# Kernel tuning notes

Measured on AMD Instinct MI355X. Metric: run time of the kernel, lower is better.

The kernel has to match this reference:

```python
import jax, jax.numpy as jnp
import numpy as np
from jax import lax

B, T, D = 16, 1024, 512
L_ORDER, R_ORDER = 1, 1
THRESHOLD = 1.0
SMOOTH = 1.0
NOISE = 0.0
TAIL = 0.45


def setup_inputs() -> dict:
    key = jax.random.key(0)
    k1, k2, k3, k4, k5 = jax.random.split(key, 5)
    hidden = jax.random.normal(k1, (B, T, D), dtype=jnp.float32)
    mask = jnp.ones((B, 1, T), dtype=jnp.float32)
    conv_w = jax.random.normal(k2, (D, 1, L_ORDER + R_ORDER + 1), dtype=jnp.float32) * 0.05
    conv_b = jax.random.normal(k3, (D,), dtype=jnp.float32) * 0.05
    lin_w = jax.random.normal(k4, (D,), dtype=jnp.float32) * 0.05
    lin_b = jax.random.normal(k5, (1,), dtype=jnp.float32) * 0.05
    return {"hidden": hidden, "mask": mask, "conv_w": conv_w, "conv_b": conv_b,
            "lin_w": lin_w, "lin_b": lin_b}


def _cif(hidden, alphas, threshold):
    # hidden [B, T1, D], alphas [B, T1]
    b, t1, d = hidden.shape

    def step(carry, xs):
        integrate, frame = carry          # [B], [B, D]
        alpha, h_t = xs                   # [B], [B, D]
        dist = 1.0 - integrate
        integrate = integrate + alpha
        fires_t = integrate
        fire = integrate >= threshold
        integrate = jnp.where(fire, integrate - 1.0, integrate)
        cur = jnp.where(fire, dist, alpha)
        rem = alpha - cur
        frame = frame + cur[:, None] * h_t
        frames_t = frame
        frame = jnp.where(fire[:, None], rem[:, None] * h_t, frame)
        return (integrate, frame), (fires_t, frames_t)

    init = (jnp.zeros((b,), hidden.dtype), jnp.zeros((b, d), hidden.dtype))
    xs = (jnp.swapaxes(alphas, 0, 1), jnp.swapaxes(hidden, 0, 1))
    _, (fires, frames) = lax.scan(step, init, xs)
    fires = jnp.swapaxes(fires, 0, 1)     # [B, T1]
    frames = jnp.swapaxes(frames, 0, 1)   # [B, T1, D]

    # Ragged gather of fired frames, padded to static length T1 (>= max token count).
    fire_mask = fires >= threshold
    pos = jnp.cumsum(fire_mask.astype(jnp.int32), axis=1) - 1
    pos = jnp.where(fire_mask, pos, t1)   # out-of-bounds index -> dropped
    b_idx = jnp.broadcast_to(jnp.arange(b)[:, None], (b, t1))
    acoustic = jnp.zeros((b, t1, d), hidden.dtype).at[b_idx, pos, :].set(frames, mode="drop")
    return acoustic, fires


def reference(hidden, mask, conv_w, conv_b, lin_w, lin_b):
    # depthwise conv branch: context [B, D, T]
    ctx = jnp.swapaxes(hidden, 1, 2)
    padded = jnp.pad(ctx, ((0, 0), (0, 0), (L_ORDER, R_ORDER)))
    memory = lax.conv_general_dilated(
        padded, conv_w, window_strides=(1,), padding="VALID",
        dimension_numbers=("NCH", "OIH", "NCH"), feature_group_count=D)
    memory = memory + conv_b[None, :, None]
    out = jax.nn.relu(jnp.swapaxes(memory + ctx, 1, 2))  # [B, T, D]
    logits = jnp.einsum("btd,d->bt", out, lin_w) + lin_b[0]
    alphas = jax.nn.sigmoid(logits)
    alphas = jax.nn.relu(alphas * SMOOTH - NOISE)
    m = mask[:, 0, :]                     # [B, T]
    alphas = alphas * m

    # tail_process_fn (no target length given)
    zeros_t = jnp.zeros((B, 1), jnp.float32)
    ones_t = jnp.ones((B, 1), jnp.float32)
    mask_1 = jnp.concatenate([m, zeros_t], axis=1)
    mask_2 = jnp.concatenate([ones_t, m], axis=1)
    tail = (mask_2 - mask_1) * TAIL
    alphas2 = jnp.concatenate([alphas, zeros_t], axis=1) + tail   # [B, T+1]
    hidden2 = jnp.concatenate([hidden, jnp.zeros((B, 1, D), hidden.dtype)], axis=1)
    token_num = jnp.floor(jnp.sum(alphas2, axis=-1))

    acoustic_embeds, cif_peak = _cif(hidden2, alphas2, THRESHOLD)
    # NOTE: torch version slices acoustic_embeds[:, :max(token_num)] (data-dependent);
    # we keep the static T+1 padding, extra positions are exactly zero.
    return acoustic_embeds, token_num, alphas2, cif_peak
```

## Files before the change

### kernel.cpp

```cpp
#include <hip/hip_runtime.h>
#include <math.h>

#define BB 16
#define TT 1024
#define DD 512
#define T1 (TT + 1)
#define PS 1028
#define TAIL_C 0.45f
#define CH 8

__global__ __launch_bounds__(256) void alphas_kernel(
    const float* __restrict__ hidden, const float* __restrict__ mask,
    const float* __restrict__ conv_w, const float* __restrict__ conv_b,
    const float* __restrict__ lin_w, const float* __restrict__ lin_b,
    float* __restrict__ alphas2)
{
    const int wave = blockIdx.x * 4 + (threadIdx.x >> 6);
    const int lane = threadIdx.x & 63;
    const int b = wave / (TT / CH);
    const int c = wave % (TT / CH);
    const int t0 = c * CH;
    const int d0 = lane * 8;

    float cw[24], cb[8], lw[8];
    {
        const float4* p = (const float4*)(conv_w + (size_t)d0 * 3);
#pragma unroll
        for (int j = 0; j < 6; ++j) {
            float4 v = p[j];
            cw[j * 4 + 0] = v.x; cw[j * 4 + 1] = v.y;
            cw[j * 4 + 2] = v.z; cw[j * 4 + 3] = v.w;
        }
        float4 b0 = *(const float4*)(conv_b + d0);
        float4 b1 = *(const float4*)(conv_b + d0 + 4);
        cb[0]=b0.x; cb[1]=b0.y; cb[2]=b0.z; cb[3]=b0.w;
        cb[4]=b1.x; cb[5]=b1.y; cb[6]=b1.z; cb[7]=b1.w;
        float4 l0 = *(const float4*)(lin_w + d0);
        float4 l1 = *(const float4*)(lin_w + d0 + 4);
        lw[0]=l0.x; lw[1]=l0.y; lw[2]=l0.z; lw[3]=l0.w;
        lw[4]=l1.x; lw[5]=l1.y; lw[6]=l1.z; lw[7]=l1.w;
    }

    const float* base = hidden + (size_t)b * TT * DD + d0;

    float rows[CH + 2][8];
#pragma unroll
    for (int r = 0; r < CH + 2; ++r) {
        const int t = t0 - 1 + r;
        if (t >= 0 && t < TT) {
            float4 a  = *(const float4*)(base + (size_t)t * DD);
            float4 bq = *(const float4*)(base + (size_t)t * DD + 4);
            rows[r][0]=a.x;  rows[r][1]=a.y;  rows[r][2]=a.z;  rows[r][3]=a.w;
            rows[r][4]=bq.x; rows[r][5]=bq.y; rows[r][6]=bq.z; rows[r][7]=bq.w;
        } else {
#pragma unroll
            for (int j = 0; j < 8; ++j) rows[r][j] = 0.f;
        }
    }

    float acc[CH];
#pragma unroll
    for (int r = 0; r < CH; ++r) {
        float s = 0.f;
#pragma unroll
        for (int j = 0; j < 8; ++j) {
            float x = fmaf(cw[3*j],   rows[r][j],
                      fmaf(cw[3*j+1], rows[r+1][j],
                      fmaf(cw[3*j+2], rows[r+2][j], cb[j]))) + rows[r+1][j];
            x = fmaxf(x, 0.f);
            s = fmaf(x, lw[j], s);
        }
        acc[r] = s;
    }

#pragma unroll
    for (int r = 0; r < CH; ++r) {
#pragma unroll
        for (int off = 32; off; off >>= 1) acc[r] += __shfl_xor(acc[r], off, 64);
    }

    if (lane < CH) {
        float v = acc[0];
#pragma unroll
        for (int r = 1; r < CH; ++r) v = (lane == r) ? acc[r] : v;
        const int t = t0 + lane;
        float logit = v + lin_b[0];
        float alpha = 1.f / (1.f + expf(-logit));
        float m = mask[b * TT + t];
        float a = fmaxf(alpha, 0.f) * m;
        float m2 = (t == 0) ? 1.0f : mask[b * TT + t - 1];
        alphas2[(size_t)b * T1 + t] = a + (m2 - m) * TAIL_C;
    } else if (lane == CH && c == 0) {
        alphas2[(size_t)b * T1 + TT] = mask[b * TT + TT - 1] * TAIL_C;
    }
}

__device__ __forceinline__ void chain32(const float4* buf, float& integ,
                                        float4* out) {
#pragma unroll
    for (int j = 0; j < 8; ++j) {
        float4 v = buf[j];
        float4 o;
        float s;
        s = integ + v.x; o.x = s; asm("v_fract_f32 %0, %1" : "=v"(integ) : "v"(s));
        s = integ + v.y; o.y = s; asm("v_fract_f32 %0, %1" : "=v"(integ) : "v"(s));
        s = integ + v.z; o.z = s; asm("v_fract_f32 %0, %1" : "=v"(integ) : "v"(s));
        s = integ + v.w; o.w = s; asm("v_fract_f32 %0, %1" : "=v"(integ) : "v"(s));
        out[j] = o;
    }
}

__global__ __launch_bounds__(256) void cif_phase_a(
    const float* __restrict__ alphas2, float* __restrict__ token_num,
    float* __restrict__ cif_peak, int* __restrict__ fire_pos,
    int* __restrict__ n_fires)
{
    __shared__ float s_a[BB * PS];
    __shared__ float s_peak[BB * PS];
    const int tid = threadIdx.x;

    {
        const float4* src = (const float4*)alphas2;
        for (int i = tid; i < (BB * T1) / 4; i += 256) {
            float4 v = src[i];
            const int e = i * 4;
            int b = e / T1;
            int t = e - b * T1;
            float el[4] = {v.x, v.y, v.z, v.w};
#pragma unroll
            for (int j = 0; j < 4; ++j) {
                int bb = b, tt = t + j;
                if (tt >= T1) { bb += 1; tt -= T1; }
                s_a[bb * PS + tt] = el[j];
            }
        }
    }
    __syncthreads();

    {
        const int b = tid >> 4, i = tid & 15;
        float part = 0.f;
        for (int t = i; t < T1; t += 16) part += s_a[b * PS + t];
        part += __shfl_xor(part, 1, 64);
        part += __shfl_xor(part, 2, 64);
        part += __shfl_xor(part, 4, 64);
        part += __shfl_xor(part, 8, 64);
        if (i == 0) token_num[b] = floorf(part);
    }

    if (tid < BB) {
        const float4* sa4 = (const float4*)(s_a + tid * PS);
        float4* sp4 = (float4*)(s_peak + tid * PS);
        float4 A[8], Bv[8], OA[8], OB[8];
#pragma unroll
        for (int j = 0; j < 8; ++j) A[j] = sa4[j];
        float integ = 0.f;
        for (int c = 0; c < 32; c += 2) {
#pragma unroll
            for (int j = 0; j < 8; ++j) Bv[j] = sa4[(c + 1) * 8 + j];
            chain32(A, integ, OA);
#pragma unroll
            for (int j = 0; j < 8; ++j) sp4[c * 8 + j] = OA[j];
            if (c + 2 < 32) {
#pragma unroll
                for (int j = 0; j < 8; ++j) A[j] = sa4[(c + 2) * 8 + j];
            }
            chain32(Bv, integ, OB);
#pragma unroll
            for (int j = 0; j < 8; ++j) sp4[(c + 1) * 8 + j] = OB[j];
        }
        float s = integ + s_a[tid * PS + TT];
        s_peak[tid * PS + TT] = s;
    }
    __syncthreads();

    {
        float4* dst = (float4*)cif_peak;
        for (int i = tid; i < (BB * T1) / 4; i += 256) {
            const int e = i * 4;
            int b = e / T1;
            int t = e - b * T1;
            float4 v;
            float* pv = &v.x;
#pragma unroll
            for (int j = 0; j < 4; ++j) {
                int bb = b, tt = t + j;
                if (tt >= T1) { bb += 1; tt -= T1; }
                pv[j] = s_peak[bb * PS + tt];
            }
            dst[i] = v;
        }
    }

    {
        const int wv = tid >> 6, lane = tid & 63;
        for (int bi = 0; bi < 4; ++bi) {
            const int b = wv * 4 + bi;
            const float* sp = s_peak + b * PS;
            int k0 = 0;
            for (int base = 0; base < T1; base += 64) {
                const int t = base + lane;
                const float p = (t < T1) ? sp[t] : 0.f;
                const bool fire = (p >= 1.0f);
                unsigned long long mballot = __ballot(fire);
                if (fire) {
                    int rank = __popcll(mballot & ((1ull << lane) - 1));
                    fire_pos[b * T1 + k0 + rank] = t;
                }
                k0 += __popcll(mballot);
            }
            if (lane == 0) n_fires[b] = k0;
        }
    }
}

__global__ __launch_bounds__(256) void cif_gather(
    const float* __restrict__ hidden, const float* __restrict__ alphas2,
    const float* __restrict__ cif_peak, const int* __restrict__ fire_pos,
    const int* __restrict__ n_fires, float* __restrict__ acoustic)
{
    const int wave = blockIdx.x * 4 + (threadIdx.x >> 6);
    const int lane = threadIdx.x & 63;
    const int b = wave / T1;
    const int k = wave % T1;
    const int d0 = lane * 8;

    float4 acc0 = make_float4(0.f, 0.f, 0.f, 0.f);
    float4 acc1 = make_float4(0.f, 0.f, 0.f, 0.f);

    const int nf = n_fires[b];
    if (k < nf) {
        const int te = fire_pos[b * T1 + k];
        int ts; float wstart;
        if (k == 0) {
            ts = 0;
            wstart = alphas2[b * T1];
        } else {
            ts = fire_pos[b * T1 + k - 1];
            wstart = cif_peak[b * T1 + ts] - 1.0f;
        }
        const float ae = alphas2[b * T1 + te];
        const float wend = 1.0f - cif_peak[b * T1 + te] + ae;

        for (int t = ts; t <= te; ++t) {
            if (t >= TT) break;
            float w = (t == te) ? wend : (t == ts) ? wstart
                                       : alphas2[b * T1 + t];
            const float* hrow = hidden + (size_t)(b * TT + t) * DD + d0;
            float4 h0 = *(const float4*)hrow;
            float4 h1 = *(const float4*)(hrow + 4);
            acc0.x = fmaf(w, h0.x, acc0.x);
            acc0.y = fmaf(w, h0.y, acc0.y);
            acc0.z = fmaf(w, h0.z, acc0.z);
            acc0.w = fmaf(w, h0.w, acc0.w);
            acc1.x = fmaf(w, h1.x, acc1.x);
            acc1.y = fmaf(w, h1.y, acc1.y);
            acc1.z = fmaf(w, h1.z, acc1.z);
            acc1.w = fmaf(w, h1.w, acc1.w);
        }
    }
    float* arow = acoustic + (size_t)(b * T1 + k) * DD + d0;
    *(float4*)arow = acc0;
    *(float4*)(arow + 4) = acc1;
}

extern "C" void kernel_launch(void* const* d_in, const int* in_sizes, int n_in,
                              void* d_out, int out_size, void* d_ws, size_t ws_size,
                              hipStream_t stream) {
    const float* hidden = (const float*)d_in[0];
    const float* mask   = (const float*)d_in[1];
    const float* conv_w = (const float*)d_in[2];
    const float* conv_b = (const float*)d_in[3];
    const float* lin_w  = (const float*)d_in[4];
    const float* lin_b  = (const float*)d_in[5];

    float* out       = (float*)d_out;
    float* out_aco   = out;
    float* out_tok   = out + (size_t)BB * T1 * DD;
    float* out_alp   = out_tok + BB;
    float* out_peak  = out_alp + (size_t)BB * T1;

    int* fire_pos = (int*)d_ws;
    int* nf       = fire_pos + (size_t)BB * T1;

    alphas_kernel<<<(BB * (TT / CH)) / 4, 256, 0, stream>>>(
        hidden, mask, conv_w, conv_b, lin_w, lin_b, out_alp);

    cif_phase_a<<<1, 256, 0, stream>>>(
        out_alp, out_tok, out_peak, fire_pos, nf);

    cif_gather<<<(BB * T1) / 4, 256, 0, stream>>>(
        hidden, out_alp, out_peak, fire_pos, nf, out_aco);
}
```

Measured before the change: 124.2 us.

## Fuse three CIF kernels into one cooperative kernel with grid syncs

Merges the alpha computation, the serial CIF scan and the frame gather into one persistent cooperative kernel of 256 blocks, separated by grid-wide barriers. It also shares a single LDS buffer for alphas and peaks so the scan runs in place. This removes two kernel launch boundaries and their gaps. In exchange the middle phase runs on one block while every other block spins at the grid barrier. The persistent grid-stride loops also use fewer waves than the original launches, which may reduce latency hiding in the bandwidth-bound phases.

```diff
diff --git a/kernel.cpp b/kernel.cpp
--- a/kernel.cpp
+++ b/kernel.cpp
@@ -1,5 +1,8 @@
 #include <hip/hip_runtime.h>
+#include <hip/hip_cooperative_groups.h>
 #include <math.h>
+
+namespace cg = cooperative_groups;
 
 #define BB 16
 #define TT 1024
@@ -8,92 +11,9 @@
 #define PS 1028
 #define TAIL_C 0.45f
 #define CH 8
-
-__global__ __launch_bounds__(256) void alphas_kernel(
-    const float* __restrict__ hidden, const float* __restrict__ mask,
-    const float* __restrict__ conv_w, const float* __restrict__ conv_b,
-    const float* __restrict__ lin_w, const float* __restrict__ lin_b,
-    float* __restrict__ alphas2)
-{
-    const int wave = blockIdx.x * 4 + (threadIdx.x >> 6);
-    const int lane = threadIdx.x & 63;
-    const int b = wave / (TT / CH);
-    const int c = wave % (TT / CH);
-    const int t0 = c * CH;
-    const int d0 = lane * 8;
-
-    float cw[24], cb[8], lw[8];
-    {
-        const float4* p = (const float4*)(conv_w + (size_t)d0 * 3);
-#pragma unroll
-        for (int j = 0; j < 6; ++j) {
-            float4 v = p[j];
-            cw[j * 4 + 0] = v.x; cw[j * 4 + 1] = v.y;
-            cw[j * 4 + 2] = v.z; cw[j * 4 + 3] = v.w;
-        }
-        float4 b0 = *(const float4*)(conv_b + d0);
-        float4 b1 = *(const float4*)(conv_b + d0 + 4);
-        cb[0]=b0.x; cb[1]=b0.y; cb[2]=b0.z; cb[3]=b0.w;
-        cb[4]=b1.x; cb[5]=b1.y; cb[6]=b1.z; cb[7]=b1.w;
-        float4 l0 = *(const float4*)(lin_w + d0);
-        float4 l1 = *(const float4*)(lin_w + d0 + 4);
-        lw[0]=l0.x; lw[1]=l0.y; lw[2]=l0.z; lw[3]=l0.w;
-        lw[4]=l1.x; lw[5]=l1.y; lw[6]=l1.z; lw[7]=l1.w;
-    }
-
-    const float* base = hidden + (size_t)b * TT * DD + d0;
-
-    float rows[CH + 2][8];
-#pragma unroll
-    for (int r = 0; r < CH + 2; ++r) {
-        const int t = t0 - 1 + r;
-        if (t >= 0 && t < TT) {
-            float4 a  = *(const float4*)(base + (size_t)t * DD);
-            float4 bq = *(const float4*)(base + (size_t)t * DD + 4);
-            rows[r][0]=a.x;  rows[r][1]=a.y;  rows[r][2]=a.z;  rows[r][3]=a.w;
-            rows[r][4]=bq.x; rows[r][5]=bq.y; rows[r][6]=bq.z; rows[r][7]=bq.w;
-        } else {
-#pragma unroll
-            for (int j = 0; j < 8; ++j) rows[r][j] = 0.f;
-        }
-    }
-
-    float acc[CH];
-#pragma unroll
-    for (int r = 0; r < CH; ++r) {
-        float s = 0.f;
-#pragma unroll
-        for (int j = 0; j < 8; ++j) {
-            float x = fmaf(cw[3*j],   rows[r][j],
-                      fmaf(cw[3*j+1], rows[r+1][j],
-                      fmaf(cw[3*j+2], rows[r+2][j], cb[j]))) + rows[r+1][j];
-            x = fmaxf(x, 0.f);
-            s = fmaf(x, lw[j], s);
-        }
-        acc[r] = s;
-    }
-
-#pragma unroll
-    for (int r = 0; r < CH; ++r) {
-#pragma unroll
-        for (int off = 32; off; off >>= 1) acc[r] += __shfl_xor(acc[r], off, 64);
-    }
-
-    if (lane < CH) {
-        float v = acc[0];
-#pragma unroll
-        for (int r = 1; r < CH; ++r) v = (lane == r) ? acc[r] : v;
-        const int t = t0 + lane;
-        float logit = v + lin_b[0];
-        float alpha = 1.f / (1.f + expf(-logit));
-        float m = mask[b * TT + t];
-        float a = fmaxf(alpha, 0.f) * m;
-        float m2 = (t == 0) ? 1.0f : mask[b * TT + t - 1];
-        alphas2[(size_t)b * T1 + t] = a + (m2 - m) * TAIL_C;
-    } else if (lane == CH && c == 0) {
-        alphas2[(size_t)b * T1 + TT] = mask[b * TT + TT - 1] * TAIL_C;
-    }
-}
+#define NBLK 256
+#define NTHR 256
+#define NWAVES (NBLK * (NTHR / 64))
 
 __device__ __forceinline__ void chain32(const float4* buf, float& integ,
                                         float4* out) {
@@ -110,158 +30,243 @@
     }
 }
 
-__global__ __launch_bounds__(256) void cif_phase_a(
-    const float* __restrict__ alphas2, float* __restrict__ token_num,
-    float* __restrict__ cif_peak, int* __restrict__ fire_pos,
-    int* __restrict__ n_fires)
+__global__ __launch_bounds__(NTHR) void cif_fused(
+    const float* __restrict__ hidden, const float* __restrict__ mask,
+    const float* __restrict__ conv_w, const float* __restrict__ conv_b,
+    const float* __restrict__ lin_w, const float* __restrict__ lin_b,
+    float* __restrict__ acoustic, float* __restrict__ token_num,
+    float* __restrict__ alphas2, float* __restrict__ cif_peak,
+    int* __restrict__ fire_pos, int* __restrict__ n_fires)
 {
-    __shared__ float s_a[BB * PS];
-    __shared__ float s_peak[BB * PS];
+    cg::grid_group grid = cg::this_grid();
+    __shared__ float s_buf[BB * PS];
+
     const int tid = threadIdx.x;
-
-    {
-        const float4* src = (const float4*)alphas2;
-        for (int i = tid; i < (BB * T1) / 4; i += 256) {
-            float4 v = src[i];
-            const int e = i * 4;
-            int b = e / T1;
-            int t = e - b * T1;
-            float el[4] = {v.x, v.y, v.z, v.w};
-#pragma unroll
-            for (int j = 0; j < 4; ++j) {
-                int bb = b, tt = t + j;
-                if (tt >= T1) { bb += 1; tt -= T1; }
-                s_a[bb * PS + tt] = el[j];
-            }
-        }
-    }
-    __syncthreads();
-
-    {
-        const int b = tid >> 4, i = tid & 15;
-        float part = 0.f;
-        for (int t = i; t < T1; t += 16) part += s_a[b * PS + t];
-        part += __shfl_xor(part, 1, 64);
-        part += __shfl_xor(part, 2, 64);
-        part += __shfl_xor(part, 4, 64);
-        part += __shfl_xor(part, 8, 64);
-        if (i == 0) token_num[b] = floorf(part);
-    }
-
-    if (tid < BB) {
-        const float4* sa4 = (const float4*)(s_a + tid * PS);
-        float4* sp4 = (float4*)(s_peak + tid * PS);
-        float4 A[8], Bv[8], OA[8], OB[8];
-#pragma unroll
-        for (int j = 0; j < 8; ++j) A[j] = sa4[j];
-        float integ = 0.f;
-        for (int c = 0; c < 32; c += 2) {
-#pragma unroll
-            for (int j = 0; j < 8; ++j) Bv[j] = sa4[(c + 1) * 8 + j];
-            chain32(A, integ, OA);
-#pragma unroll
-            for (int j = 0; j < 8; ++j) sp4[c * 8 + j] = OA[j];
-            if (c + 2 < 32) {
-#pragma unroll
-                for (int j = 0; j < 8; ++j) A[j] = sa4[(c + 2) * 8 + j];
-            }
-            chain32(Bv, integ, OB);
-#pragma unroll
-            for (int j = 0; j < 8; ++j) sp4[(c + 1) * 8 + j] = OB[j];
-        }
-        float s = integ + s_a[tid * PS + TT];
-        s_peak[tid * PS + TT] = s;
-    }
-    __syncthreads();
-
-    {
-        float4* dst = (float4*)cif_peak;
-        for (int i = tid; i < (BB * T1) / 4; i += 256) {
-            const int e = i * 4;
-            int b = e / T1;
-            int t = e - b * T1;
-            float4 v;
-            float* pv = &v.x;
-#pragma unroll
-            for (int j = 0; j < 4; ++j) {
-                int bb = b, tt = t + j;
-                if (tt >= T1) { bb += 1; tt -= T1; }
-                pv[j] = s_peak[bb * PS + tt];
-            }
-            dst[i] = v;
-        }
-    }
-
-    {
-        const int wv = tid >> 6, lane = tid & 63;
-        for (int bi = 0; bi < 4; ++bi) {
-            const int b = wv * 4 + bi;
-            const float* sp = s_peak + b * PS;
-            int k0 = 0;
-            for (int base = 0; base < T1; base += 64) {
-                const int t = base + lane;
-                const float p = (t < T1) ? sp[t] : 0.f;
-                const bool fire = (p >= 1.0f);
-                unsigned long long mballot = __ballot(fire);
-                if (fire) {
-                    int rank = __popcll(mballot & ((1ull << lane) - 1));
-                    fire_pos[b * T1 + k0 + rank] = t;
-                }
-                k0 += __popcll(mballot);
-            }
-            if (lane == 0) n_fires[b] = k0;
-        }
-    }
-}
-
-__global__ __launch_bounds__(256) void cif_gather(
-    const float* __restrict__ hidden, const float* __restrict__ alphas2,
-    const float* __restrict__ cif_peak, const int* __restrict__ fire_pos,
-    const int* __restrict__ n_fires, float* __restrict__ acoustic)
-{
-    const int wave = blockIdx.x * 4 + (threadIdx.x >> 6);
-    const int lane = threadIdx.x & 63;
-    const int b = wave / T1;
-    const int k = wave % T1;
-    const int d0 = lane * 8;
-
-    float4 acc0 = make_float4(0.f, 0.f, 0.f, 0.f);
-    float4 acc1 = make_float4(0.f, 0.f, 0.f, 0.f);
-
-    const int nf = n_fires[b];
-    if (k < nf) {
-        const int te = fire_pos[b * T1 + k];
-        int ts; float wstart;
-        if (k == 0) {
-            ts = 0;
-            wstart = alphas2[b * T1];
-        } else {
-            ts = fire_pos[b * T1 + k - 1];
-            wstart = cif_peak[b * T1 + ts] - 1.0f;
-        }
-        const float ae = alphas2[b * T1 + te];
-        const float wend = 1.0f - cif_peak[b * T1 + te] + ae;
-
-        for (int t = ts; t <= te; ++t) {
-            if (t >= TT) break;
-            float w = (t == te) ? wend : (t == ts) ? wstart
-                                       : alphas2[b * T1 + t];
-            const float* hrow = hidden + (size_t)(b * TT + t) * DD + d0;
-            float4 h0 = *(const float4*)hrow;
-            float4 h1 = *(const float4*)(hrow + 4);
-            acc0.x = fmaf(w, h0.x, acc0.x);
-            acc0.y = fmaf(w, h0.y, acc0.y);
-            acc0.z = fmaf(w, h0.z, acc0.z);
-            acc0.w = fmaf(w, h0.w, acc0.w);
-            acc1.x = fmaf(w, h1.x, acc1.x);
-            acc1.y = fmaf(w, h1.y, acc1.y);
-            acc1.z = fmaf(w, h1.z, acc1.z);
-            acc1.w = fmaf(w, h1.w, acc1.w);
-        }
-    }
-    float* arow = acoustic + (size_t)(b * T1 + k) * DD + d0;
-    *(float4*)arow = acc0;
-    *(float4*)(arow + 4) = acc1;
+    const int lane = tid & 63;
+    const int gwave = blockIdx.x * (NTHR / 64) + (tid >> 6);
+
+    for (int task = gwave; task < BB * (TT / CH); task += NWAVES) {
+        const int b = task / (TT / CH);
+        const int c = task % (TT / CH);
+        const int t0 = c * CH;
+        const int d0 = lane * 8;
+
+        float cw[24], cb[8], lw[8];
+        {
+            const float4* p = (const float4*)(conv_w + (size_t)d0 * 3);
+#pragma unroll
+            for (int j = 0; j < 6; ++j) {
+                float4 v = p[j];
+                cw[j * 4 + 0] = v.x; cw[j * 4 + 1] = v.y;
+                cw[j * 4 + 2] = v.z; cw[j * 4 + 3] = v.w;
+            }
+            float4 b0 = *(const float4*)(conv_b + d0);
+            float4 b1 = *(const float4*)(conv_b + d0 + 4);
+            cb[0]=b0.x; cb[1]=b0.y; cb[2]=b0.z; cb[3]=b0.w;
+            cb[4]=b1.x; cb[5]=b1.y; cb[6]=b1.z; cb[7]=b1.w;
+            float4 l0 = *(const float4*)(lin_w + d0);
+            float4 l1 = *(const float4*)(lin_w + d0 + 4);
+            lw[0]=l0.x; lw[1]=l0.y; lw[2]=l0.z; lw[3]=l0.w;
+            lw[4]=l1.x; lw[5]=l1.y; lw[6]=l1.z; lw[7]=l1.w;
+        }
+
+        const float* base = hidden + (size_t)b * TT * DD + d0;
+
+        float rows[CH + 2][8];
+#pragma unroll
+        for (int r = 0; r < CH + 2; ++r) {
+            const int t = t0 - 1 + r;
+            if (t >= 0 && t < TT) {
+                float4 a  = *(const float4*)(base + (size_t)t * DD);
+                float4 bq = *(const float4*)(base + (size_t)t * DD + 4);
+                rows[r][0]=a.x;  rows[r][1]=a.y;  rows[r][2]=a.z;  rows[r][3]=a.w;
+                rows[r][4]=bq.x; rows[r][5]=bq.y; rows[r][6]=bq.z; rows[r][7]=bq.w;
+            } else {
+#pragma unroll
+                for (int j = 0; j < 8; ++j) rows[r][j] = 0.f;
+            }
+        }
+
+        float acc[CH];
+#pragma unroll
+        for (int r = 0; r < CH; ++r) {
+            float s = 0.f;
+#pragma unroll
+            for (int j = 0; j < 8; ++j) {
+                float x = fmaf(cw[3*j],   rows[r][j],
+                          fmaf(cw[3*j+1], rows[r+1][j],
+                          fmaf(cw[3*j+2], rows[r+2][j], cb[j]))) + rows[r+1][j];
+                x = fmaxf(x, 0.f);
+                s = fmaf(x, lw[j], s);
+            }
+            acc[r] = s;
+        }
+
+#pragma unroll
+        for (int r = 0; r < CH; ++r) {
+#pragma unroll
+            for (int off = 32; off; off >>= 1) acc[r] += __shfl_xor(acc[r], off, 64);
+        }
+
+        if (lane < CH) {
+            float v = acc[0];
+#pragma unroll
+            for (int r = 1; r < CH; ++r) v = (lane == r) ? acc[r] : v;
+            const int t = t0 + lane;
+            float logit = v + lin_b[0];
+            float alpha = 1.f / (1.f + expf(-logit));
+            float m = mask[b * TT + t];
+            float a = fmaxf(alpha, 0.f) * m;
+            float m2 = (t == 0) ? 1.0f : mask[b * TT + t - 1];
+            alphas2[(size_t)b * T1 + t] = a + (m2 - m) * TAIL_C;
+        } else if (lane == CH && c == 0) {
+            alphas2[(size_t)b * T1 + TT] = mask[b * TT + TT - 1] * TAIL_C;
+        }
+    }
+
+    grid.sync();
+
+    if (blockIdx.x == 0) {
+        {
+            const float4* src = (const float4*)alphas2;
+            for (int i = tid; i < (BB * T1) / 4; i += NTHR) {
+                float4 v = src[i];
+                const int e = i * 4;
+                int b = e / T1;
+                int t = e - b * T1;
+                float el[4] = {v.x, v.y, v.z, v.w};
+#pragma unroll
+                for (int j = 0; j < 4; ++j) {
+                    int bb = b, tt = t + j;
+                    if (tt >= T1) { bb += 1; tt -= T1; }
+                    s_buf[bb * PS + tt] = el[j];
+                }
+            }
+        }
+        __syncthreads();
+
+        {
+            const int b = tid >> 4, i = tid & 15;
+            float part = 0.f;
+            for (int t = i; t < T1; t += 16) part += s_buf[b * PS + t];
+            part += __shfl_xor(part, 1, 64);
+            part += __shfl_xor(part, 2, 64);
+            part += __shfl_xor(part, 4, 64);
+            part += __shfl_xor(part, 8, 64);
+            if (i == 0) token_num[b] = floorf(part);
+        }
+        __syncthreads();
+
+        if (tid < BB) {
+            float4* sb4 = (float4*)(s_buf + tid * PS);
+            float4 A[8], Bv[8], OA[8], OB[8];
+#pragma unroll
+            for (int j = 0; j < 8; ++j) A[j] = sb4[j];
+            float integ = 0.f;
+            for (int c = 0; c < 32; c += 2) {
+#pragma unroll
+                for (int j = 0; j < 8; ++j) Bv[j] = sb4[(c + 1) * 8 + j];
+                chain32(A, integ, OA);
+#pragma unroll
+                for (int j = 0; j < 8; ++j) sb4[c * 8 + j] = OA[j];
+                if (c + 2 < 32) {
+#pragma unroll
+                    for (int j = 0; j < 8; ++j) A[j] = sb4[(c + 2) * 8 + j];
+                }
+                chain32(Bv, integ, OB);
+#pragma unroll
+                for (int j = 0; j < 8; ++j) sb4[(c + 1) * 8 + j] = OB[j];
+            }
+            float s = integ + s_buf[tid * PS + TT];
+            s_buf[tid * PS + TT] = s;
+        }
+        __syncthreads();
+
+        {
+            float4* dst = (float4*)cif_peak;
+            for (int i = tid; i < (BB * T1) / 4; i += NTHR) {
+                const int e = i * 4;
+                int b = e / T1;
+                int t = e - b * T1;
+                float4 v;
+                float* pv = &v.x;
+#pragma unroll
+                for (int j = 0; j < 4; ++j) {
+                    int bb = b, tt = t + j;
+                    if (tt >= T1) { bb += 1; tt -= T1; }
+                    pv[j] = s_buf[bb * PS + tt];
+                }
+                dst[i] = v;
+            }
+        }
+
+        {
+            const int wv = tid >> 6;
+            for (int bi = 0; bi < 4; ++bi) {
+                const int b = wv * 4 + bi;
+                const float* sp = s_buf + b * PS;
+                int k0 = 0;
+                for (int base = 0; base < T1; base += 64) {
+                    const int t = base + lane;
+                    const float p = (t < T1) ? sp[t] : 0.f;
+                    const bool fire = (p >= 1.0f);
+                    unsigned long long mb = __ballot(fire);
+                    if (fire) {
+                        int rank = __popcll(mb & ((1ull << lane) - 1));
+                        fire_pos[b * T1 + k0 + rank] = t;
+                    }
+                    k0 += __popcll(mb);
+                }
+                if (lane == 0) n_fires[b] = k0;
+            }
+        }
+    }
+
+    grid.sync();
+
+    for (int task = gwave; task < BB * T1; task += NWAVES) {
+        const int b = task / T1;
+        const int k = task % T1;
+        const int d0 = lane * 8;
+
+        float4 acc0 = make_float4(0.f, 0.f, 0.f, 0.f);
+        float4 acc1 = make_float4(0.f, 0.f, 0.f, 0.f);
+
+        const int nf = n_fires[b];
+        if (k < nf) {
+            const int te = fire_pos[b * T1 + k];
+            int ts; float wstart;
+            if (k == 0) {
+                ts = 0;
+                wstart = alphas2[b * T1];
+            } else {
+                ts = fire_pos[b * T1 + k - 1];
+                wstart = cif_peak[b * T1 + ts] - 1.0f;
+            }
+            const float ae = alphas2[b * T1 + te];
+            const float wend = 1.0f - cif_peak[b * T1 + te] + ae;
+
+            for (int t = ts; t <= te; ++t) {
+                if (t >= TT) break;
+                float w = (t == te) ? wend : (t == ts) ? wstart
+                                           : alphas2[b * T1 + t];
+                const float* hrow = hidden + (size_t)(b * TT + t) * DD + d0;
+                float4 h0 = *(const float4*)hrow;
+                float4 h1 = *(const float4*)(hrow + 4);
+                acc0.x = fmaf(w, h0.x, acc0.x);
+                acc0.y = fmaf(w, h0.y, acc0.y);
+                acc0.z = fmaf(w, h0.z, acc0.z);
+                acc0.w = fmaf(w, h0.w, acc0.w);
+                acc1.x = fmaf(w, h1.x, acc1.x);
+                acc1.y = fmaf(w, h1.y, acc1.y);
+                acc1.z = fmaf(w, h1.z, acc1.z);
+                acc1.w = fmaf(w, h1.w, acc1.w);
+            }
+        }
+        float* arow = acoustic + (size_t)(b * T1 + k) * DD + d0;
+        *(float4*)arow = acc0;
+        *(float4*)(arow + 4) = acc1;
+    }
 }
 
 extern "C" void kernel_launch(void* const* d_in, const int* in_sizes, int n_in,
@@ -283,12 +288,12 @@
     int* fire_pos = (int*)d_ws;
     int* nf       = fire_pos + (size_t)BB * T1;
 
-    alphas_kernel<<<(BB * (TT / CH)) / 4, 256, 0, stream>>>(
-        hidden, mask, conv_w, conv_b, lin_w, lin_b, out_alp);
-
-    cif_phase_a<<<1, 256, 0, stream>>>(
-        out_alp, out_tok, out_peak, fire_pos, nf);
-
-    cif_gather<<<(BB * T1) / 4, 256, 0, stream>>>(
-        hidden, out_alp, out_peak, fire_pos, nf, out_aco);
+    void* args[] = {
+        (void*)&hidden, (void*)&mask, (void*)&conv_w, (void*)&conv_b,
+        (void*)&lin_w, (void*)&lin_b,
+        (void*)&out_aco, (void*)&out_tok, (void*)&out_alp, (void*)&out_peak,
+        (void*)&fire_pos, (void*)&nf
+    };
+    hipLaunchCooperativeKernel((const void*)cif_fused, dim3(NBLK), dim3(NTHR),
+                               args, 0, stream);
 }
```

Result: slower. 204.1 us (+64.3%).

## Prefetch hidden into cache with helper blocks while the serial CIF chain runs

Applied to the files above, without the earlier changes.

The single-block CIF phase becomes a 257-block kernel. Block 0 runs the serial integrate-and-fire chain, now using one shared buffer instead of two. The other 256 blocks stream slices of `hidden` to warm the L2/MALL cache for the later gather kernel, and stop once block 0 sets a completion flag in the workspace. The flag is never reset inside the kernel, so on repeated calls the prefetch may be skipped, and the extra reads compete for memory bandwidth.

```diff
diff --git a/kernel.cpp b/kernel.cpp
--- a/kernel.cpp
+++ b/kernel.cpp
@@ -8,6 +8,10 @@
 #define PS 1028
 #define TAIL_C 0.45f
 #define CH 8
+
+#define WS_FLAG 0
+#define WS_SINK 1
+#define WS_FP   4
 
 __global__ __launch_bounds__(256) void alphas_kernel(
     const float* __restrict__ hidden, const float* __restrict__ mask,
@@ -110,14 +114,33 @@
     }
 }
 
-__global__ __launch_bounds__(256) void cif_phase_a(
-    const float* __restrict__ alphas2, float* __restrict__ token_num,
-    float* __restrict__ cif_peak, int* __restrict__ fire_pos,
-    int* __restrict__ n_fires)
+__global__ __launch_bounds__(256) void cif_chain(
+    const float* __restrict__ alphas2, const float* __restrict__ hidden,
+    float* __restrict__ token_num, float* __restrict__ cif_peak,
+    int* __restrict__ ws)
 {
-    __shared__ float s_a[BB * PS];
-    __shared__ float s_peak[BB * PS];
+    __shared__ float s_buf[BB * PS];
     const int tid = threadIdx.x;
+
+    if (blockIdx.x != 0) {
+        const int bid = blockIdx.x - 1;
+        const size_t slice = (size_t)BB * TT * DD / 4 / 256;
+        const float4* p = (const float4*)hidden + (size_t)bid * slice;
+        float s = 0.f;
+        for (int pass = 0; pass < 24; ++pass) {
+            if (__hip_atomic_load(&ws[WS_FLAG], __ATOMIC_RELAXED,
+                                  __HIP_MEMORY_SCOPE_AGENT) == 1) break;
+            for (int i = tid; i < (int)slice; i += 256) {
+                float4 v = p[i];
+                s += v.x + v.y + v.z + v.w;
+            }
+        }
+        if (s == 1.2345678e38f) ((float*)ws)[WS_SINK] = s;
+        return;
+    }
+
+    int* fire_pos = ws + WS_FP;
+    int* n_fires  = ws + WS_FP + BB * T1;
 
     {
         const float4* src = (const float4*)alphas2;
@@ -131,7 +154,7 @@
             for (int j = 0; j < 4; ++j) {
                 int bb = b, tt = t + j;
                 if (tt >= T1) { bb += 1; tt -= T1; }
-                s_a[bb * PS + tt] = el[j];
+                s_buf[bb * PS + tt] = el[j];
             }
         }
     }
@@ -140,37 +163,37 @@
     {
         const int b = tid >> 4, i = tid & 15;
         float part = 0.f;
-        for (int t = i; t < T1; t += 16) part += s_a[b * PS + t];
+        for (int t = i; t < T1; t += 16) part += s_buf[b * PS + t];
         part += __shfl_xor(part, 1, 64);
         part += __shfl_xor(part, 2, 64);
         part += __shfl_xor(part, 4, 64);
         part += __shfl_xor(part, 8, 64);
         if (i == 0) token_num[b] = floorf(part);
     }
+    __syncthreads();
 
     if (tid < BB) {
-        const float4* sa4 = (const float4*)(s_a + tid * PS);
-        float4* sp4 = (float4*)(s_peak + tid * PS);
+        float4* sb4 = (float4*)(s_buf + tid * PS);
         float4 A[8], Bv[8], OA[8], OB[8];
 #pragma unroll
-        for (int j = 0; j < 8; ++j) A[j] = sa4[j];
+        for (int j = 0; j < 8; ++j) A[j] = sb4[j];
         float integ = 0.f;
         for (int c = 0; c < 32; c += 2) {
 #pragma unroll
-            for (int j = 0; j < 8; ++j) Bv[j] = sa4[(c + 1) * 8 + j];
+            for (int j = 0; j < 8; ++j) Bv[j] = sb4[(c + 1) * 8 + j];
             chain32(A, integ, OA);
 #pragma unroll
-            for (int j = 0; j < 8; ++j) sp4[c * 8 + j] = OA[j];
+            for (int j = 0; j < 8; ++j) sb4[c * 8 + j] = OA[j];
             if (c + 2 < 32) {
 #pragma unroll
-                for (int j = 0; j < 8; ++j) A[j] = sa4[(c + 2) * 8 + j];
+                for (int j = 0; j < 8; ++j) A[j] = sb4[(c + 2) * 8 + j];
             }
             chain32(Bv, integ, OB);
 #pragma unroll
-            for (int j = 0; j < 8; ++j) sp4[(c + 1) * 8 + j] = OB[j];
-        }
-        float s = integ + s_a[tid * PS + TT];
-        s_peak[tid * PS + TT] = s;
+            for (int j = 0; j < 8; ++j) sb4[(c + 1) * 8 + j] = OB[j];
+        }
+        float s = integ + s_buf[tid * PS + TT];
+        s_buf[tid * PS + TT] = s;
     }
     __syncthreads();
 
@@ -186,7 +209,7 @@
             for (int j = 0; j < 4; ++j) {
                 int bb = b, tt = t + j;
                 if (tt >= T1) { bb += 1; tt -= T1; }
-                pv[j] = s_peak[bb * PS + tt];
+                pv[j] = s_buf[bb * PS + tt];
             }
             dst[i] = v;
         }
@@ -196,29 +219,36 @@
         const int wv = tid >> 6, lane = tid & 63;
         for (int bi = 0; bi < 4; ++bi) {
             const int b = wv * 4 + bi;
-            const float* sp = s_peak + b * PS;
+            const float* sp = s_buf + b * PS;
             int k0 = 0;
             for (int base = 0; base < T1; base += 64) {
                 const int t = base + lane;
                 const float p = (t < T1) ? sp[t] : 0.f;
                 const bool fire = (p >= 1.0f);
-                unsigned long long mballot = __ballot(fire);
+                unsigned long long mb = __ballot(fire);
                 if (fire) {
-                    int rank = __popcll(mballot & ((1ull << lane) - 1));
+                    int rank = __popcll(mb & ((1ull << lane) - 1));
                     fire_pos[b * T1 + k0 + rank] = t;
                 }
-                k0 += __popcll(mballot);
+                k0 += __popcll(mb);
             }
             if (lane == 0) n_fires[b] = k0;
         }
     }
+    __syncthreads();
+    if (tid == 0)
+        __hip_atomic_store(&ws[WS_FLAG], 1, __ATOMIC_RELEASE,
+                           __HIP_MEMORY_SCOPE_AGENT);
 }
 
 __global__ __launch_bounds__(256) void cif_gather(
     const float* __restrict__ hidden, const float* __restrict__ alphas2,
-    const float* __restrict__ cif_peak, const int* __restrict__ fire_pos,
-    const int* __restrict__ n_fires, float* __restrict__ acoustic)
+    const float* __restrict__ cif_peak, const int* __restrict__ ws,
+    float* __restrict__ acoustic)
 {
+    const int* fire_pos = ws + WS_FP;
+    const int* n_fires  = ws + WS_FP + BB * T1;
+
     const int wave = blockIdx.x * 4 + (threadIdx.x >> 6);
     const int lane = threadIdx.x & 63;
     const int b = wave / T1;
@@ -280,15 +310,14 @@
     float* out_alp   = out_tok + BB;
     float* out_peak  = out_alp + (size_t)BB * T1;
 
-    int* fire_pos = (int*)d_ws;
-    int* nf       = fire_pos + (size_t)BB * T1;
+    int* wsI = (int*)d_ws;
 
     alphas_kernel<<<(BB * (TT / CH)) / 4, 256, 0, stream>>>(
         hidden, mask, conv_w, conv_b, lin_w, lin_b, out_alp);
 
-    cif_phase_a<<<1, 256, 0, stream>>>(
-        out_alp, out_tok, out_peak, fire_pos, nf);
+    cif_chain<<<257, 256, 0, stream>>>(
+        out_alp, hidden, out_tok, out_peak, wsI);
 
     cif_gather<<<(BB * T1) / 4, 256, 0, stream>>>(
-        hidden, out_alp, out_peak, fire_pos, nf, out_aco);
-}
+        hidden, out_alp, out_peak, wsI, out_aco);
+}
```

New measurement: 128.0 us. 3.1% more time.
